# Performance work log

Hardware: AMD Instinct MI355X
Metric: run time of the kernel (lower is better)

Reference implementation:

```python
import jax, jax.numpy as jnp
import numpy as np

D_EQUI = 64
D_INV = 256
D_MSG = 64
N_HEADS = 32
D_HEAD = D_INV // N_HEADS
D_FF = 256
D_EDGE_IN = 64
D_EDGE_OUT = 64
D_OUT = D_EQUI + N_HEADS + D_EDGE_OUT  # 160
IN_FEATS = 2 * D_MSG + D_EQUI + D_EDGE_IN  # 256
B, N = 4, 256


def setup_inputs() -> dict:
    key = jax.random.key(0)
    ks = jax.random.split(key, 20)
    s = 0.05
    inp = {
        "equis": jax.random.normal(ks[0], (B, N, 3, D_EQUI), jnp.float32),
        "invs": jax.random.normal(ks[1], (B, N, D_INV), jnp.float32),
        "edges": jax.random.normal(ks[2], (B, N, N, D_EDGE_IN), jnp.float32),
        "adj_matrix": jnp.ones((B, N, N), jnp.int32),
        # _PairwiseMessages params
        "qW": jax.random.normal(ks[3], (D_INV, D_MSG), jnp.float32) * s,
        "qb": jnp.zeros((D_MSG,), jnp.float32),
        "kW": jax.random.normal(ks[4], (D_INV, D_MSG), jnp.float32) * s,
        "kb": jnp.zeros((D_MSG,), jnp.float32),
        "mW1": jax.random.normal(ks[5], (IN_FEATS, D_FF), jnp.float32) * s,
        "mb1": jnp.zeros((D_FF,), jnp.float32),
        "mW2": jax.random.normal(ks[6], (D_FF, D_OUT), jnp.float32) * s,
        "mb2": jnp.zeros((D_OUT,), jnp.float32),
        # _InvAttention params
        "inv_inW": jax.random.normal(ks[7], (D_INV, D_INV), jnp.float32) * s,
        "inv_inb": jnp.zeros((D_INV,), jnp.float32),
        "inv_outW": jax.random.normal(ks[8], (D_INV, D_INV), jnp.float32) * s,
        "inv_outb": jnp.zeros((D_INV,), jnp.float32),
        # _EquiAttention params (no bias)
        "equi_inW": jax.random.normal(ks[9], (D_EQUI, D_EQUI), jnp.float32) * s,
        "equi_outW": jax.random.normal(ks[10], (D_EQUI, D_EQUI), jnp.float32) * s,
    }
    return inp


def _forward(equis, invs, edges, adj_matrix, qW, qb, kW, kb, mW1, mb1, mW2, mb2,
             inv_inW, inv_inb, inv_outW, inv_outb, equi_inW, equi_outW):
    # ---- pairwise messages ----
    # dotprods of equivariant 3-vectors per channel: [B, Nq, Nk, d_equi]
    dot = jnp.einsum("bqdc,bkdc->bqkc", equis, equis)
    qm = invs @ qW + qb  # [B,N,d_msg]
    km = invs @ kW + kb
    Nn = invs.shape[1]
    feats = jnp.concatenate([
        jnp.broadcast_to(qm[:, :, None, :], (qm.shape[0], Nn, Nn, D_MSG)),
        jnp.broadcast_to(km[:, None, :, :], (km.shape[0], Nn, Nn, D_MSG)),
        dot,
        edges,
    ], axis=-1)  # [B,N,N,in_feats]
    msgs = jax.nn.silu(feats @ mW1 + mb1) @ mW2 + mb2  # [B,N,N,d_out]

    # adjacency -> additive mask (0 where connected, -inf otherwise)
    mask = jnp.where(adj_matrix == 0, -jnp.inf, 0.0).astype(msgs.dtype)

    # ---- invariant attention (first n_heads channels) ----
    inv_msgs = msgs[..., :N_HEADS] + mask[..., None]
    attn_i = jax.nn.softmax(inv_msgs, axis=2)  # softmax over kv
    hf = (invs @ inv_inW + inv_inb).reshape(invs.shape[0], Nn, N_HEADS, D_HEAD)
    out_i = jnp.einsum("bqkh,bkhd->bqhd", attn_i, hf)
    w_i = jnp.sqrt(jnp.sum(attn_i * attn_i, axis=2))  # [B,q,H]
    out_i = out_i * w_i[..., None]
    inv_updates = out_i.reshape(invs.shape[0], Nn, D_INV) @ inv_outW + inv_outb

    # ---- equivariant attention (next d_equi channels) ----
    equi_msgs = msgs[..., N_HEADS:N_HEADS + D_EQUI] + mask[..., None]
    attn_e = jax.nn.softmax(equi_msgs, axis=2)  # [B,q,k,c]
    pe = equis @ equi_inW  # [B,N,3,d_equi]
    out_e = jnp.einsum("bqkc,bkdc->bqdc", attn_e, pe)
    w_e = jnp.sqrt(jnp.sum(attn_e * attn_e, axis=2))  # [B,q,c]
    out_e = out_e * w_e[:, :, None, :]
    equi_updates = out_e @ equi_outW  # [B,N,3,d_equi]

    # ---- edge updates (remaining channels) ----
    edge_updates = msgs[..., N_HEADS + D_EQUI:]
    return equi_updates, inv_updates, edge_updates


def reference(equis, invs, edges, adj_matrix, qW, qb, kW, kb, mW1, mb1, mW2, mb2,
              inv_inW, inv_inb, inv_outW, inv_outb, equi_inW, equi_outW):
    return _forward(equis, invs, edges, adj_matrix, qW, qb, kW, kb, mW1, mb1, mW2, mb2,
                    inv_inW, inv_inb, inv_outW, inv_outb, equi_inW, equi_outW)
```

## Files before the change

### kernel.cpp

```cpp
#include <hip/hip_runtime.h>
#include <hip/hip_bf16.h>
#include <math.h>


typedef __attribute__((ext_vector_type(8))) short short8;
typedef __attribute__((ext_vector_type(8))) __bf16 bf16x8;
typedef __attribute__((ext_vector_type(4))) float f32x4;

constexpr int EQUI_OFF = 0;
constexpr int INV_OFF  = 196608;
constexpr int EDGE_OFF = 458752;

__device__ __forceinline__ unsigned short f2bf(float x) {
    unsigned u = __builtin_bit_cast(unsigned, x);
    u = u + 0x7FFFu + ((u >> 16) & 1u);
    return (unsigned short)(u >> 16);
}
__device__ __forceinline__ float bf2f(unsigned short u) {
    return __builtin_bit_cast(float, ((unsigned)u) << 16);
}
__device__ __forceinline__ unsigned short f2bfh(float x) {
    return __builtin_bit_cast(unsigned short, (__bf16)x);
}
__device__ __forceinline__ unsigned pk2(float a, float b) {
    return (unsigned)f2bfh(a) | ((unsigned)f2bfh(b) << 16);
}
__device__ __forceinline__ short8 pk8(f32x4 a, f32x4 b) {
    bf16x8 r = { (__bf16)a.x, (__bf16)a.y, (__bf16)a.z, (__bf16)a.w,
                 (__bf16)b.x, (__bf16)b.y, (__bf16)b.z, (__bf16)b.w };
    return __builtin_bit_cast(short8, r);
}
__device__ __forceinline__ f32x4 MFMA(short8 a, short8 b, f32x4 c) {
    return __builtin_amdgcn_mfma_f32_16x16x32_bf16(
        __builtin_bit_cast(bf16x8, a), __builtin_bit_cast(bf16x8, b), c, 0, 0, 0);
}

__global__ void prep1(const float* __restrict__ invs, const float* __restrict__ equis,
                      const float* __restrict__ qW, const float* __restrict__ qb,
                      const float* __restrict__ kW, const float* __restrict__ kb,
                      const float* __restrict__ inv_inW, const float* __restrict__ inv_inb,
                      const float* __restrict__ equi_inW,
                      const float* __restrict__ mW1, const float* __restrict__ mW2,
                      float* __restrict__ qm, float* __restrict__ km,
                      float* __restrict__ hf, float* __restrict__ pe,
                      short* __restrict__ W1T, short* __restrict__ W2T) {
    int tid = threadIdx.x, bi = blockIdx.x;
    if (bi < 1024) {
        int r = bi;
        __shared__ float sInv[256];
        sInv[tid] = invs[r * 256 + tid];
        __syncthreads();
        if (tid < 64) {
            float acc = qb[tid];
            for (int f = 0; f < 256; ++f) acc += sInv[f] * qW[f * 64 + tid];
            qm[r * 64 + tid] = acc;
        } else if (tid < 128) {
            int c = tid - 64;
            float acc = kb[c];
            for (int f = 0; f < 256; ++f) acc += sInv[f] * kW[f * 64 + c];
            km[r * 64 + c] = acc;
        }
        float acch = inv_inb[tid];
        for (int f = 0; f < 256; ++f) acch += sInv[f] * inv_inW[f * 256 + tid];
        hf[r * 256 + tid] = acch;
    } else if (bi < 2048) {
        int rn = bi - 1024;
        if (tid < 192) {
            int d = tid >> 6, c = tid & 63;
            const float* erow = equis + (size_t)rn * 192 + d * 64;
            float acc = 0.f;
            for (int f = 0; f < 64; ++f) acc += erow[f] * equi_inW[f * 64 + c];
            pe[rn * 192 + d * 64 + c] = acc;
        }
    } else {
        int idx = (bi - 2048) * 256 + tid;
        if (idx < 32768) {
            int n = idx >> 7, kk = idx & 127;
            W1T[idx] = (short)f2bf(mW1[(128 + kk) * 256 + n]);
        } else {
            int i2 = idx - 32768;
            int n = i2 >> 8, f = i2 & 255;
            W2T[i2] = (short)f2bf(mW2[f * 160 + n]);
        }
    }
}

__global__ void prep2(const float* __restrict__ qm, const float* __restrict__ km,
                      const float* __restrict__ mW1, const float* __restrict__ mb1,
                      const float* __restrict__ hf, const float* __restrict__ pe,
                      const float* __restrict__ inv_outW, const float* __restrict__ equi_outW,
                      float* __restrict__ c1, float* __restrict__ c2,
                      unsigned short* __restrict__ hfT, unsigned short* __restrict__ peT,
                      unsigned short* __restrict__ WoT, unsigned short* __restrict__ EoT) {
    __shared__ float sT[64][65];
    int tid = threadIdx.x, bi = blockIdx.x;
    if (bi < 1024) {
        int r = bi;
        if (tid < 64) sT[0][tid] = qm[r * 64 + tid];
        __syncthreads();
        float acc = mb1[tid];
        #pragma unroll 8
        for (int k = 0; k < 64; ++k) acc = fmaf(sT[0][k], mW1[k * 256 + tid], acc);
        c1[r * 256 + tid] = acc;
    } else if (bi < 2048) {
        int r = bi - 1024;
        if (tid < 64) sT[0][tid] = km[r * 64 + tid];
        __syncthreads();
        float acc = 0.f;
        #pragma unroll 8
        for (int k = 0; k < 64; ++k) acc = fmaf(sT[0][k], mW1[(64 + k) * 256 + tid], acc);
        c2[r * 256 + tid] = acc;
    } else {
        int bt = bi - 2048;
        if (bt < 64) {
            int b = bt >> 4, t = bt & 15, tj = t >> 2, th = t & 3;
            #pragma unroll
            for (int i = 0; i < 16; ++i) { int idx = i * 256 + tid; int jl = idx >> 6, hl = idx & 63;
                sT[jl][hl] = hf[((size_t)(b * 256 + tj * 64 + jl)) * 256 + th * 64 + hl]; }
            __syncthreads();
            #pragma unroll
            for (int i = 0; i < 16; ++i) { int idx = i * 256 + tid; int hl = idx >> 6, jl = idx & 63;
                hfT[((size_t)(b * 256 + th * 64 + hl)) * 256 + tj * 64 + jl] = f2bf(sT[jl][hl]); }
        } else if (bt < 128) {
            int i2 = bt - 64; int b = i2 >> 4, t = i2 & 15, tj = t >> 2, d = t & 3;
            if (d == 3) {
                #pragma unroll
                for (int i = 0; i < 16; ++i) { int idx = i * 256 + tid; int c = idx >> 6, jl = idx & 63;
                    peT[((size_t)((b * 64 + c) * 4 + 3)) * 256 + tj * 64 + jl] = 0; }
            } else {
                #pragma unroll
                for (int i = 0; i < 16; ++i) { int idx = i * 256 + tid; int jl = idx >> 6, c = idx & 63;
                    sT[jl][c] = pe[((size_t)(b * 256 + tj * 64 + jl)) * 192 + d * 64 + c]; }
                __syncthreads();
                #pragma unroll
                for (int i = 0; i < 16; ++i) { int idx = i * 256 + tid; int c = idx >> 6, jl = idx & 63;
                    peT[((size_t)((b * 64 + c) * 4 + d)) * 256 + tj * 64 + jl] = f2bf(sT[jl][c]); }
            }
        } else if (bt < 144) {
            int i2 = bt - 128; int tf = i2 >> 2, tn = i2 & 3;
            #pragma unroll
            for (int i = 0; i < 16; ++i) { int idx = i * 256 + tid; int fl = idx >> 6, nl = idx & 63;
                sT[fl][nl] = inv_outW[(size_t)(tf * 64 + fl) * 256 + tn * 64 + nl]; }
            __syncthreads();
            #pragma unroll
            for (int i = 0; i < 16; ++i) { int idx = i * 256 + tid; int nl = idx >> 6, fl = idx & 63;
                WoT[(size_t)(tn * 64 + nl) * 256 + tf * 64 + fl] = f2bf(sT[fl][nl]); }
        } else {
            #pragma unroll
            for (int i = 0; i < 16; ++i) { int idx = i * 256 + tid; int cl = idx >> 6, c2i = idx & 63;
                sT[cl][c2i] = equi_outW[cl * 64 + c2i]; }
            __syncthreads();
            #pragma unroll
            for (int i = 0; i < 16; ++i) { int idx = i * 256 + tid; int c2i = idx >> 6, cl = idx & 63;
                EoT[c2i * 64 + cl] = f2bf(sT[cl][c2i]); }
        }
    }
}

constexpr int GA_AH   = 0;
constexpr int GA_EQ   = 32768;
constexpr int GA_MASK = 33536;
constexpr int GA_BYTES = 33792;

__launch_bounds__(256, 4)
__global__ void semla_gemm(const float* __restrict__ equis, const float* __restrict__ edges,
                           const int* __restrict__ adj, const float* __restrict__ mb2,
                           const short* __restrict__ W1T, const short* __restrict__ W2T,
                           const float* __restrict__ c1, const float* __restrict__ c2,
                           float* __restrict__ out, unsigned short* __restrict__ PT) {
    extern __shared__ char smem[];
    float* sEQ   = (float*)(smem + GA_EQ);
    float* sMask = (float*)(smem + GA_MASK);

    const int tid  = threadIdx.x;
    const int lane = tid & 63;
    const int w    = tid >> 6;
    const int bid  = blockIdx.x;
    const int bq   = bid >> 2;
    const int jc   = bid & 3;
    const int b    = bq >> 8;

    const int lrow = lane & 15;
    const int kgrp = (lane >> 4) << 3;
    const int drow = (lane >> 4) << 2;

    if (tid < 192) sEQ[tid] = equis[(size_t)bq * 192 + tid];
    if (tid < 64)  sMask[tid] = adj[(size_t)bq * 256 + (jc << 6) + tid] ? 0.f : -1e30f;

    float c1v[4];
    #pragma unroll
    for (int ni = 0; ni < 4; ++ni)
        c1v[ni] = c1[bq * 256 + (w << 6) + (ni << 4) + lrow];
    const int ntiles = (w < 2) ? 3 : 2;
    const int nbase  = (w < 2) ? w * 48 : 96 + (w - 2) * 32;
    float b2v[3];
    #pragma unroll
    for (int ti = 0; ti < 3; ++ti)
        if (ti < ntiles) b2v[ti] = mb2[nbase + (ti << 4) + lrow];

    auto stA16 = [&](int row, int colbyte, short8 v) {
        int byte = ((row << 8) + colbyte) ^ ((row & 7) << 4);
        *(short8*)(smem + GA_AH + byte) = v;
    };
    auto ldA = [&](int row, int kb) -> short8 {
        int byte = ((row << 8) + (kb << 1)) ^ ((row & 7) << 4);
        return *(const short8*)(smem + GA_AH + byte);
    };
    auto stH = [&](int row, int col, unsigned short v) {
        int byte = ((row << 9) + (col << 1)) ^ ((row & 7) << 4);
        *(unsigned short*)(smem + GA_AH + byte) = v;
    };
    auto ldH = [&](int row, int kb) -> short8 {
        int byte = ((row << 9) + (kb << 1)) ^ ((row & 7) << 4);
        return *(const short8*)(smem + GA_AH + byte);
    };

    __syncthreads();

    {
        int r = tid >> 2, h = tid & 3;
        const float* erow = equis + (size_t)((b << 8) + (jc << 6) + r) * 192;
        #pragma unroll
        for (int g = 0; g < 2; ++g) {
            int cg = h + g * 4;
            f32x4 lo = (f32x4)(0.f), hi = (f32x4)(0.f);
            #pragma unroll
            for (int d = 0; d < 3; ++d) {
                f32x4 e0 = *(const f32x4*)(erow + d * 64 + cg * 8);
                f32x4 e1 = *(const f32x4*)(erow + d * 64 + cg * 8 + 4);
                f32x4 q0 = *(const f32x4*)(sEQ + d * 64 + cg * 8);
                f32x4 q1 = *(const f32x4*)(sEQ + d * 64 + cg * 8 + 4);
                lo += e0 * q0; hi += e1 * q1;
            }
            stA16(r, cg * 16, pk8(lo, hi));
        }
        const float* ebase = edges + ((size_t)bq * 256 + (jc << 6)) * 64;
        #pragma unroll
        for (int g = 0; g < 2; ++g) {
            int c8 = h + g * 4;
            f32x4 e0 = *(const f32x4*)(ebase + r * 64 + c8 * 8);
            f32x4 e1 = *(const f32x4*)(ebase + r * 64 + c8 * 8 + 4);
            stA16(r, 128 + c8 * 16, pk8(e0, e1));
        }
    }
    __syncthreads();

    f32x4 acc[4][4];
    #pragma unroll
    for (int mi = 0; mi < 4; ++mi)
        #pragma unroll
        for (int ni = 0; ni < 4; ++ni) acc[mi][ni] = (f32x4)(0.f);

    #pragma unroll
    for (int k0 = 0; k0 < 128; k0 += 32) {
        int kb = k0 + kgrp;
        short8 a0 = ldA(lrow, kb), a1 = ldA(16 + lrow, kb),
               a2 = ldA(32 + lrow, kb), a3 = ldA(48 + lrow, kb);
        short8 bf[4];
        #pragma unroll
        for (int ni = 0; ni < 4; ++ni)
            bf[ni] = *(const short8*)(W1T + ((w << 6) + (ni << 4) + lrow) * 128 + kb);
        #pragma unroll
        for (int ni = 0; ni < 4; ++ni) {
            acc[0][ni] = MFMA(a0, bf[ni], acc[0][ni]);
            acc[1][ni] = MFMA(a1, bf[ni], acc[1][ni]);
            acc[2][ni] = MFMA(a2, bf[ni], acc[2][ni]);
            acc[3][ni] = MFMA(a3, bf[ni], acc[3][ni]);
        }
    }
    __syncthreads();

    const float* c2base = c2 + ((size_t)((b << 8) + (jc << 6)) << 8);
    #pragma unroll
    for (int mi = 0; mi < 4; ++mi)
        #pragma unroll
        for (int r = 0; r < 4; ++r) {
            int row = (mi << 4) + drow + r;
            const float* c2row = c2base + (row << 8);
            #pragma unroll
            for (int ni = 0; ni < 4; ++ni) {
                int n = (w << 6) + (ni << 4) + lrow;
                float x = acc[mi][ni][r] + c1v[ni] + c2row[n];
                float hh = x * __builtin_amdgcn_rcpf(1.f + __expf(-x));
                stH(row, n, f2bfh(hh));
            }
        }
    __syncthreads();

    f32x4 acc2[4][3];
    #pragma unroll
    for (int mi = 0; mi < 4; ++mi)
        #pragma unroll
        for (int ti = 0; ti < 3; ++ti) acc2[mi][ti] = (f32x4)(0.f);

    #pragma unroll
    for (int k0 = 0; k0 < 256; k0 += 32) {
        int kb = k0 + kgrp;
        short8 a0 = ldH(lrow, kb), a1 = ldH(16 + lrow, kb),
               a2 = ldH(32 + lrow, kb), a3 = ldH(48 + lrow, kb);
        short8 bt[3];
        #pragma unroll
        for (int ti = 0; ti < 3; ++ti)
            if (ti < ntiles) bt[ti] = *(const short8*)(W2T + (nbase + (ti << 4) + lrow) * 256 + kb);
        #pragma unroll
        for (int ti = 0; ti < 3; ++ti)
            if (ti < ntiles) {
                acc2[0][ti] = MFMA(a0, bt[ti], acc2[0][ti]);
                acc2[1][ti] = MFMA(a1, bt[ti], acc2[1][ti]);
                acc2[2][ti] = MFMA(a2, bt[ti], acc2[2][ti]);
                acc2[3][ti] = MFMA(a3, bt[ti], acc2[3][ti]);
            }
    }
    __syncthreads();

    if (w < 2) {
        #pragma unroll
        for (int ti = 0; ti < 3; ++ti) {
            int n = nbase + (ti << 4) + lrow;
            float bias = b2v[ti];
            #pragma unroll
            for (int mi = 0; mi < 4; ++mi) {
                int j0 = (mi << 4) + drow;
                f32x4 mv = *(const f32x4*)(sMask + j0);
                unsigned lo = pk2(acc2[mi][ti][0] + bias + mv.x,
                                  acc2[mi][ti][1] + bias + mv.y);
                unsigned hi = pk2(acc2[mi][ti][2] + bias + mv.z,
                                  acc2[mi][ti][3] + bias + mv.w);
                *(unsigned*)(smem + n * 136 + j0 * 2)     = lo;
                *(unsigned*)(smem + n * 136 + j0 * 2 + 4) = hi;
            }
        }
    } else {
        #pragma unroll
        for (int mi = 0; mi < 4; ++mi)
            #pragma unroll
            for (int ti = 0; ti < 2; ++ti) {
                int n = nbase + (ti << 4) + lrow;
                #pragma unroll
                for (int r = 0; r < 4; ++r) {
                    int j = (jc << 6) + (mi << 4) + drow + r;
                    out[EDGE_OFF + ((size_t)bq * 256 + j) * 64 + (n - 96)] = acc2[mi][ti][r] + b2v[ti];
                }
            }
    }
    __syncthreads();

    if (tid < 192) {
        int n = tid >> 1, half = tid & 1;
        const char* src = smem + n * 136 + half * 64;
        unsigned short* dst = PT + (((size_t)bq * 96 + n) << 8) + (jc << 6) + half * 32;
        #pragma unroll
        for (int i = 0; i < 4; ++i)
            *(short8*)(dst + i * 8) = *(const short8*)(src + i * 16);
    }
}

constexpr int ES_A = 0;
constexpr int ES_W = 32768;
constexpr int ES_BYTES = 33024;

__launch_bounds__(256, 4)
__global__ void semla_einsum(const unsigned short* __restrict__ PT,
                             const unsigned short* __restrict__ hfT,
                             const unsigned short* __restrict__ peT,
                             unsigned short* __restrict__ OIb, unsigned short* __restrict__ OEb) {
    extern __shared__ char smem[];
    float* sW = (float*)(smem + ES_W);
    const int tid = threadIdx.x, lane = tid & 63, w = tid >> 6;
    const int bi = blockIdx.x;
    const int qc = bi & 3;
    const int t  = bi >> 2;
    const int b  = t / 96;
    const int c  = t - 96 * b;
    const int lrow = lane & 15, kgrp = (lane >> 4) << 3, drow = (lane >> 4) << 2;

    #pragma unroll
    for (int i = 0; i < 8; ++i) {
        int id = i * 256 + tid; int row = id >> 5, ck = id & 31;
        size_t src = (((size_t)((b << 8) + (qc << 6) + row) * 96 + c) << 8) + ck * 16;
        short8 v = *(const short8*)(PT + src);
        int byte = ((row << 9) + (ck << 4)) ^ ((row & 7) << 4);
        *(short8*)(smem + ES_A + byte) = v;
    }
    __syncthreads();

    {
        int r = tid >> 2, p = tid & 3;
        float v[64];
        #pragma unroll
        for (int i = 0; i < 8; ++i) {
            int ck = p * 8 + i;
            int byte = ((r << 9) + (ck << 4)) ^ ((r & 7) << 4);
            short8 x = *(const short8*)(smem + ES_A + byte);
            #pragma unroll
            for (int e = 0; e < 8; ++e) v[i * 8 + e] = bf2f((unsigned short)x[e]);
        }
        float m = v[0];
        #pragma unroll
        for (int i = 1; i < 64; ++i) m = fmaxf(m, v[i]);
        m = fmaxf(m, __shfl_xor(m, 1)); m = fmaxf(m, __shfl_xor(m, 2));
        float s = 0.f, q = 0.f;
        #pragma unroll
        for (int i = 0; i < 64; ++i) { float e = __expf(v[i] - m); v[i] = e; s += e; q = fmaf(e, e, q); }
        s += __shfl_xor(s, 1); s += __shfl_xor(s, 2);
        q += __shfl_xor(q, 1); q += __shfl_xor(q, 2);
        float rs = (s > 0.f) ? 1.f / s : 0.f;
        if (p == 0) sW[r] = sqrtf(q) * rs;
        #pragma unroll
        for (int i = 0; i < 8; ++i) {
            int ck = p * 8 + i;
            short8 o;
            #pragma unroll
            for (int e = 0; e < 8; ++e) o[e] = (short)f2bfh(v[i * 8 + e] * rs);
            int byte = ((r << 9) + (ck << 4)) ^ ((r & 7) << 4);
            *(short8*)(smem + ES_A + byte) = o;
        }
    }
    __syncthreads();

    const unsigned short* Bbase =
        (c < 32) ? hfT + (((size_t)((b << 8) + (c << 3) + (lrow & 7))) << 8)
                 : peT + (((size_t)((((b << 6) + (c - 32)) << 2) + (lrow & 3))) << 8);
    f32x4 acc = (f32x4)(0.f);
    #pragma unroll
    for (int k0 = 0; k0 < 256; k0 += 32) {
        int kb = k0 + kgrp;
        int byte = ((((w << 4) + lrow) << 9) + (kb << 1)) ^ ((lrow & 7) << 4);
        short8 a = *(const short8*)(smem + ES_A + byte);
        short8 bb = *(const short8*)(Bbase + kb);
        acc = MFMA(a, bb, acc);
    }
    const int nvalid = (c < 32) ? 8 : 3;
    if (lrow < nvalid) {
        #pragma unroll
        for (int r2 = 0; r2 < 4; ++r2) {
            int ql = (w << 4) + drow + r2;
            float val = acc[r2] * sW[ql];
            size_t grow = (size_t)((b << 8) + (qc << 6) + ql);
            if (c < 32) OIb[(grow << 8) + (c << 3) + lrow] = f2bfh(val);
            else        OEb[(grow * 3 + lrow) * 64 + (c - 32)] = f2bfh(val);
        }
    }
}

constexpr int PJ_BYTES = 32768;

__launch_bounds__(256, 4)
__global__ void semla_proj(const unsigned short* __restrict__ OIb,
                           const unsigned short* __restrict__ OEb,
                           const unsigned short* __restrict__ WoT,
                           const unsigned short* __restrict__ EoT,
                           const float* __restrict__ inv_outb, float* __restrict__ out) {
    extern __shared__ char smem[];
    const int tid = threadIdx.x, lane = tid & 63, w = tid >> 6;
    const int lrow = lane & 15, kgrp = (lane >> 4) << 3, drow = (lane >> 4) << 2;
    const int bi = blockIdx.x;

    if (bi < 32) {
        const int mb = bi >> 1, nb = bi & 1;
        #pragma unroll
        for (int i = 0; i < 8; ++i) {
            int id = i * 256 + tid; int row = id >> 5, ck = id & 31;
            short8 v = *(const short8*)(OIb + (((size_t)(mb * 64 + row)) << 8) + ck * 16);
            int byte = ((row << 9) + (ck << 4)) ^ ((row & 7) << 4);
            *(short8*)(smem + byte) = v;
        }
        __syncthreads();
        f32x4 acc[4][2];
        #pragma unroll
        for (int mi = 0; mi < 4; ++mi)
            #pragma unroll
            for (int ti = 0; ti < 2; ++ti) acc[mi][ti] = (f32x4)(0.f);
        #pragma unroll
        for (int k0 = 0; k0 < 256; k0 += 32) {
            int kb = k0 + kgrp;
            short8 a[4];
            #pragma unroll
            for (int mi = 0; mi < 4; ++mi) {
                int byte = ((((mi << 4) + lrow) << 9) + (kb << 1)) ^ ((lrow & 7) << 4);
                a[mi] = *(const short8*)(smem + byte);
            }
            #pragma unroll
            for (int ti = 0; ti < 2; ++ti) {
                int n = nb * 128 + w * 32 + (ti << 4) + lrow;
                short8 bb = *(const short8*)(WoT + n * 256 + kb);
                #pragma unroll
                for (int mi = 0; mi < 4; ++mi) acc[mi][ti] = MFMA(a[mi], bb, acc[mi][ti]);
            }
        }
        #pragma unroll
        for (int ti = 0; ti < 2; ++ti) {
            int n = nb * 128 + w * 32 + (ti << 4) + lrow;
            float bias = inv_outb[n];
            #pragma unroll
            for (int mi = 0; mi < 4; ++mi)
                #pragma unroll
                for (int r = 0; r < 4; ++r) {
                    int row = mb * 64 + (mi << 4) + drow + r;
                    out[INV_OFF + (size_t)row * 256 + n] = acc[mi][ti][r] + bias;
                }
        }
    } else {
        const int mb = bi - 32;
        #pragma unroll
        for (int i = 0; i < 2; ++i) {
            int id = i * 256 + tid; int row = id >> 3, ck = id & 7;
            short8 v = *(const short8*)(OEb + (((size_t)(mb * 64 + row)) << 6) + ck * 16);
            int byte = ((row << 7) + (ck << 4)) ^ ((row & 7) << 4);
            *(short8*)(smem + byte) = v;
        }
        __syncthreads();
        f32x4 acc[4];
        #pragma unroll
        for (int ni = 0; ni < 4; ++ni) acc[ni] = (f32x4)(0.f);
        #pragma unroll
        for (int k0 = 0; k0 < 64; k0 += 32) {
            int kb = k0 + kgrp;
            int byte = ((((w << 4) + lrow) << 7) + (kb << 1)) ^ ((lrow & 7) << 4);
            short8 a = *(const short8*)(smem + byte);
            #pragma unroll
            for (int ni = 0; ni < 4; ++ni) {
                short8 bb = *(const short8*)(EoT + ((ni << 4) + lrow) * 64 + kb);
                acc[ni] = MFMA(a, bb, acc[ni]);
            }
        }
        #pragma unroll
        for (int ni = 0; ni < 4; ++ni)
            #pragma unroll
            for (int r = 0; r < 4; ++r) {
                int rowg = mb * 64 + (w << 4) + drow + r;
                int bq = rowg / 3, d = rowg - 3 * bq;
                out[EQUI_OFF + (size_t)bq * 192 + d * 64 + (ni << 4) + lrow] = acc[ni][r];
            }
    }
}

extern "C" void kernel_launch(void* const* d_in, const int* in_sizes, int n_in,
                              void* d_out, int out_size, void* d_ws, size_t ws_size,
                              hipStream_t stream) {
    const float* equis    = (const float*)d_in[0];
    const float* invs     = (const float*)d_in[1];
    const float* edges    = (const float*)d_in[2];
    const int*   adj      = (const int*)d_in[3];
    const float* qW       = (const float*)d_in[4];
    const float* qb       = (const float*)d_in[5];
    const float* kW       = (const float*)d_in[6];
    const float* kb       = (const float*)d_in[7];
    const float* mW1      = (const float*)d_in[8];
    const float* mb1      = (const float*)d_in[9];
    const float* mW2      = (const float*)d_in[10];
    const float* mb2      = (const float*)d_in[11];
    const float* inv_inW  = (const float*)d_in[12];
    const float* inv_inb  = (const float*)d_in[13];
    const float* inv_outW = (const float*)d_in[14];
    const float* inv_outb = (const float*)d_in[15];
    const float* equi_inW = (const float*)d_in[16];
    const float* equi_outW= (const float*)d_in[17];

    char* ws = (char*)d_ws;
    short* W1T = (short*)(ws + 0);
    short* W2T = (short*)(ws + 65536);
    float* qm  = (float*)(ws + 147456);
    float* km  = (float*)(ws + 409600);
    float* hf  = (float*)(ws + 671744);
    float* pe  = (float*)(ws + 1720320);
    float* c1  = (float*)(ws + 2506752);
    float* c2  = (float*)(ws + 3555328);
    unsigned short* PT  = (unsigned short*)(ws + 4603904);
    unsigned short* peT = (unsigned short*)(ws + 54935552);
    unsigned short* hfT = (unsigned short*)(ws + 55459840);
    unsigned short* OIb = (unsigned short*)(ws + 55984128);
    unsigned short* OEb = (unsigned short*)(ws + 56508416);
    unsigned short* WoT = (unsigned short*)(ws + 56901632);
    unsigned short* EoT = (unsigned short*)(ws + 57032704);

    prep1<<<2336, 256, 0, stream>>>(invs, equis, qW, qb, kW, kb,
                                    inv_inW, inv_inb, equi_inW, mW1, mW2,
                                    qm, km, hf, pe, W1T, W2T);
    prep2<<<2193, 256, 0, stream>>>(qm, km, mW1, mb1, hf, pe, inv_outW, equi_outW,
                                    c1, c2, hfT, peT, WoT, EoT);
    semla_gemm<<<4096, 256, GA_BYTES, stream>>>(equis, edges, adj, mb2, W1T, W2T,
                                                c1, c2, (float*)d_out, PT);
    semla_einsum<<<1536, 256, ES_BYTES, stream>>>(PT, hfT, peT, OIb, OEb);
    semla_proj<<<80, 256, PJ_BYTES, stream>>>(OIb, OEb, WoT, EoT, inv_outb, (float*)d_out);
}
```

Baseline: 161.0 us.

## Split semla_gemm tile across 8 waves with 2x4 wave grid

Doubles the block size of the fused MLP GEMM kernel from 256 to 512 threads, arranging waves as a 2x4 grid so each wave computes half the rows (32 instead of 64) of the 64-row tile. Per-wave accumulator registers are halved, and launch bounds target higher occupancy, to improve latency hiding. In exchange, weight fragments from W1T/W2T are loaded by twice as many waves per block, which increases global/L2 traffic for B operands.

```diff
diff --git a/kernel.cpp b/kernel.cpp
--- a/kernel.cpp
+++ b/kernel.cpp
@@ -162,7 +162,7 @@
 constexpr int GA_MASK = 33536;
 constexpr int GA_BYTES = 33792;
 
-__launch_bounds__(256, 4)
+__launch_bounds__(512, 6)
 __global__ void semla_gemm(const float* __restrict__ equis, const float* __restrict__ edges,
                            const int* __restrict__ adj, const float* __restrict__ mb2,
                            const short* __restrict__ W1T, const short* __restrict__ W2T,
@@ -175,6 +175,8 @@
     const int tid  = threadIdx.x;
     const int lane = tid & 63;
     const int w    = tid >> 6;
+    const int wm   = w >> 2;
+    const int wn   = w & 3;
     const int bid  = blockIdx.x;
     const int bq   = bid >> 2;
     const int jc   = bid & 3;
@@ -190,9 +192,9 @@
     float c1v[4];
     #pragma unroll
     for (int ni = 0; ni < 4; ++ni)
-        c1v[ni] = c1[bq * 256 + (w << 6) + (ni << 4) + lrow];
-    const int ntiles = (w < 2) ? 3 : 2;
-    const int nbase  = (w < 2) ? w * 48 : 96 + (w - 2) * 32;
+        c1v[ni] = c1[bq * 256 + (wn << 6) + (ni << 4) + lrow];
+    const int ntiles = (wn < 2) ? 3 : 2;
+    const int nbase  = (wn < 2) ? wn * 48 : 96 + (wn - 2) * 32;
     float b2v[3];
     #pragma unroll
     for (int ti = 0; ti < 3; ++ti)
@@ -218,68 +220,55 @@
     __syncthreads();
 
     {
-        int r = tid >> 2, h = tid & 3;
+        int r = tid >> 3, h = tid & 7;
         const float* erow = equis + (size_t)((b << 8) + (jc << 6) + r) * 192;
-        #pragma unroll
-        for (int g = 0; g < 2; ++g) {
-            int cg = h + g * 4;
-            f32x4 lo = (f32x4)(0.f), hi = (f32x4)(0.f);
-            #pragma unroll
-            for (int d = 0; d < 3; ++d) {
-                f32x4 e0 = *(const f32x4*)(erow + d * 64 + cg * 8);
-                f32x4 e1 = *(const f32x4*)(erow + d * 64 + cg * 8 + 4);
-                f32x4 q0 = *(const f32x4*)(sEQ + d * 64 + cg * 8);
-                f32x4 q1 = *(const f32x4*)(sEQ + d * 64 + cg * 8 + 4);
-                lo += e0 * q0; hi += e1 * q1;
-            }
-            stA16(r, cg * 16, pk8(lo, hi));
-        }
+        f32x4 lo = (f32x4)(0.f), hi = (f32x4)(0.f);
+        #pragma unroll
+        for (int d = 0; d < 3; ++d) {
+            f32x4 e0 = *(const f32x4*)(erow + d * 64 + h * 8);
+            f32x4 e1 = *(const f32x4*)(erow + d * 64 + h * 8 + 4);
+            f32x4 q0 = *(const f32x4*)(sEQ + d * 64 + h * 8);
+            f32x4 q1 = *(const f32x4*)(sEQ + d * 64 + h * 8 + 4);
+            lo += e0 * q0; hi += e1 * q1;
+        }
+        stA16(r, h * 16, pk8(lo, hi));
         const float* ebase = edges + ((size_t)bq * 256 + (jc << 6)) * 64;
-        #pragma unroll
-        for (int g = 0; g < 2; ++g) {
-            int c8 = h + g * 4;
-            f32x4 e0 = *(const f32x4*)(ebase + r * 64 + c8 * 8);
-            f32x4 e1 = *(const f32x4*)(ebase + r * 64 + c8 * 8 + 4);
-            stA16(r, 128 + c8 * 16, pk8(e0, e1));
-        }
-    }
-    __syncthreads();
-
-    f32x4 acc[4][4];
-    #pragma unroll
-    for (int mi = 0; mi < 4; ++mi)
+        f32x4 e0 = *(const f32x4*)(ebase + r * 64 + h * 8);
+        f32x4 e1 = *(const f32x4*)(ebase + r * 64 + h * 8 + 4);
+        stA16(r, 128 + h * 16, pk8(e0, e1));
+    }
+    __syncthreads();
+
+    f32x4 acc[2][4];
+    #pragma unroll
+    for (int mi = 0; mi < 2; ++mi)
         #pragma unroll
         for (int ni = 0; ni < 4; ++ni) acc[mi][ni] = (f32x4)(0.f);
 
     #pragma unroll
     for (int k0 = 0; k0 < 128; k0 += 32) {
         int kb = k0 + kgrp;
-        short8 a0 = ldA(lrow, kb), a1 = ldA(16 + lrow, kb),
-               a2 = ldA(32 + lrow, kb), a3 = ldA(48 + lrow, kb);
-        short8 bf[4];
-        #pragma unroll
-        for (int ni = 0; ni < 4; ++ni)
-            bf[ni] = *(const short8*)(W1T + ((w << 6) + (ni << 4) + lrow) * 128 + kb);
+        int rb = (wm << 5) + lrow;
+        short8 a0 = ldA(rb, kb), a1 = ldA(rb + 16, kb);
         #pragma unroll
         for (int ni = 0; ni < 4; ++ni) {
-            acc[0][ni] = MFMA(a0, bf[ni], acc[0][ni]);
-            acc[1][ni] = MFMA(a1, bf[ni], acc[1][ni]);
-            acc[2][ni] = MFMA(a2, bf[ni], acc[2][ni]);
-            acc[3][ni] = MFMA(a3, bf[ni], acc[3][ni]);
+            short8 bf = *(const short8*)(W1T + ((wn << 6) + (ni << 4) + lrow) * 128 + kb);
+            acc[0][ni] = MFMA(a0, bf, acc[0][ni]);
+            acc[1][ni] = MFMA(a1, bf, acc[1][ni]);
         }
     }
     __syncthreads();
 
     const float* c2base = c2 + ((size_t)((b << 8) + (jc << 6)) << 8);
     #pragma unroll
-    for (int mi = 0; mi < 4; ++mi)
+    for (int mi = 0; mi < 2; ++mi)
         #pragma unroll
         for (int r = 0; r < 4; ++r) {
-            int row = (mi << 4) + drow + r;
+            int row = (wm << 5) + (mi << 4) + drow + r;
             const float* c2row = c2base + (row << 8);
             #pragma unroll
             for (int ni = 0; ni < 4; ++ni) {
-                int n = (w << 6) + (ni << 4) + lrow;
+                int n = (wn << 6) + (ni << 4) + lrow;
                 float x = acc[mi][ni][r] + c1v[ni] + c2row[n];
                 float hh = x * __builtin_amdgcn_rcpf(1.f + __expf(-x));
                 stH(row, n, f2bfh(hh));
@@ -287,40 +276,35 @@
         }
     __syncthreads();
 
-    f32x4 acc2[4][3];
-    #pragma unroll
-    for (int mi = 0; mi < 4; ++mi)
+    f32x4 acc2[2][3];
+    #pragma unroll
+    for (int mi = 0; mi < 2; ++mi)
         #pragma unroll
         for (int ti = 0; ti < 3; ++ti) acc2[mi][ti] = (f32x4)(0.f);
 
     #pragma unroll
     for (int k0 = 0; k0 < 256; k0 += 32) {
         int kb = k0 + kgrp;
-        short8 a0 = ldH(lrow, kb), a1 = ldH(16 + lrow, kb),
-               a2 = ldH(32 + lrow, kb), a3 = ldH(48 + lrow, kb);
-        short8 bt[3];
-        #pragma unroll
-        for (int ti = 0; ti < 3; ++ti)
-            if (ti < ntiles) bt[ti] = *(const short8*)(W2T + (nbase + (ti << 4) + lrow) * 256 + kb);
+        int rb = (wm << 5) + lrow;
+        short8 a0 = ldH(rb, kb), a1 = ldH(rb + 16, kb);
         #pragma unroll
         for (int ti = 0; ti < 3; ++ti)
             if (ti < ntiles) {
-                acc2[0][ti] = MFMA(a0, bt[ti], acc2[0][ti]);
-                acc2[1][ti] = MFMA(a1, bt[ti], acc2[1][ti]);
-                acc2[2][ti] = MFMA(a2, bt[ti], acc2[2][ti]);
-                acc2[3][ti] = MFMA(a3, bt[ti], acc2[3][ti]);
-            }
-    }
-    __syncthreads();
-
-    if (w < 2) {
+                short8 bt = *(const short8*)(W2T + (nbase + (ti << 4) + lrow) * 256 + kb);
+                acc2[0][ti] = MFMA(a0, bt, acc2[0][ti]);
+                acc2[1][ti] = MFMA(a1, bt, acc2[1][ti]);
+            }
+    }
+    __syncthreads();
+
+    if (wn < 2) {
         #pragma unroll
         for (int ti = 0; ti < 3; ++ti) {
             int n = nbase + (ti << 4) + lrow;
             float bias = b2v[ti];
             #pragma unroll
-            for (int mi = 0; mi < 4; ++mi) {
-                int j0 = (mi << 4) + drow;
+            for (int mi = 0; mi < 2; ++mi) {
+                int j0 = (wm << 5) + (mi << 4) + drow;
                 f32x4 mv = *(const f32x4*)(sMask + j0);
                 unsigned lo = pk2(acc2[mi][ti][0] + bias + mv.x,
                                   acc2[mi][ti][1] + bias + mv.y);
@@ -332,13 +316,13 @@
         }
     } else {
         #pragma unroll
-        for (int mi = 0; mi < 4; ++mi)
+        for (int mi = 0; mi < 2; ++mi)
             #pragma unroll
             for (int ti = 0; ti < 2; ++ti) {
                 int n = nbase + (ti << 4) + lrow;
                 #pragma unroll
                 for (int r = 0; r < 4; ++r) {
-                    int j = (jc << 6) + (mi << 4) + drow + r;
+                    int j = (jc << 6) + (wm << 5) + (mi << 4) + drow + r;
                     out[EDGE_OFF + ((size_t)bq * 256 + j) * 64 + (n - 96)] = acc2[mi][ti][r] + b2v[ti];
                 }
             }
@@ -579,7 +563,7 @@
                                     qm, km, hf, pe, W1T, W2T);
     prep2<<<2193, 256, 0, stream>>>(qm, km, mW1, mb1, hf, pe, inv_outW, equi_outW,
                                     c1, c2, hfT, peT, WoT, EoT);
-    semla_gemm<<<4096, 256, GA_BYTES, stream>>>(equis, edges, adj, mb2, W1T, W2T,
+    semla_gemm<<<4096, 512, GA_BYTES, stream>>>(equis, edges, adj, mb2, W1T, W2T,
                                                 c1, c2, (float*)d_out, PT);
     semla_einsum<<<1536, 256, ES_BYTES, stream>>>(PT, hfT, peT, OIb, OEb);
     semla_proj<<<80, 256, PJ_BYTES, stream>>>(OIb, OEb, WoT, EoT, inv_outb, (float*)d_out);
```

Measured after the change: 237.5 us. 1.48x slower.
